# Performance work log

Hardware: AMD Instinct MI355X
Metric: run time of the kernel (lower is better)

Reference implementation:

```python
import jax, jax.numpy as jnp
import numpy as np

C, H_IMG = 1, 1024
N_PATCH = 64
L = 12          # blocks
NH = 12         # heads
D = 768         # hidden_d
DH = D // NH    # head dim
MLP = 4 * D
OUT_D = 1000
BATCH = 256
PATCH = H_IMG // N_PATCH
IN_D = C * PATCH
SEQ = N_PATCH + 1


def _pos_emb(pos, dim):
    # faithful to original: exponent uses i directly (2*i/dim), sin for even i, cos for odd i
    p = np.arange(pos, dtype=np.float64)[:, None]
    i = np.arange(dim, dtype=np.float64)[None, :]
    ang = p / np.power(10000.0, 2.0 * i / dim)
    pe = np.where((np.arange(dim)[None, :] % 2) == 0, np.sin(ang), np.cos(ang))
    return jnp.asarray(pe, dtype=jnp.float32)


def setup_inputs() -> dict:
    key = jax.random.key(0)
    ks = jax.random.split(key, 24)
    s = lambda fan: 1.0 / np.sqrt(fan)
    inp = {
        "images": jax.random.normal(ks[0], (BATCH, C, H_IMG), jnp.float32),
        "linear_w": jax.random.uniform(ks[1], (D, IN_D), jnp.float32, -s(IN_D), s(IN_D)),
        "linear_b": jax.random.uniform(ks[2], (D,), jnp.float32, -s(IN_D), s(IN_D)),
        "class_token": jax.random.uniform(ks[3], (1, D), jnp.float32),
        "pos_emb": _pos_emb(SEQ, D),
        "ln1_g": jnp.ones((L, D), jnp.float32),
        "ln1_b": jnp.zeros((L, D), jnp.float32),
        "wq": jax.random.uniform(ks[4], (L, NH, DH, DH), jnp.float32, -s(DH), s(DH)),
        "bq": jax.random.uniform(ks[5], (L, NH, DH), jnp.float32, -s(DH), s(DH)),
        "wk": jax.random.uniform(ks[6], (L, NH, DH, DH), jnp.float32, -s(DH), s(DH)),
        "bk": jax.random.uniform(ks[7], (L, NH, DH), jnp.float32, -s(DH), s(DH)),
        "wv": jax.random.uniform(ks[8], (L, NH, DH, DH), jnp.float32, -s(DH), s(DH)),
        "bv": jax.random.uniform(ks[9], (L, NH, DH), jnp.float32, -s(DH), s(DH)),
        "ln2_g": jnp.ones((L, D), jnp.float32),
        "ln2_b": jnp.zeros((L, D), jnp.float32),
        "w1": jax.random.uniform(ks[10], (L, MLP, D), jnp.float32, -s(D), s(D)),
        "b1": jax.random.uniform(ks[11], (L, MLP), jnp.float32, -s(D), s(D)),
        "w2": jax.random.uniform(ks[12], (L, D, MLP), jnp.float32, -s(MLP), s(MLP)),
        "b2": jax.random.uniform(ks[13], (L, D), jnp.float32, -s(MLP), s(MLP)),
        "head_w": jax.random.uniform(ks[14], (OUT_D, D), jnp.float32, -s(D), s(D)),
        "head_b": jax.random.uniform(ks[15], (OUT_D,), jnp.float32, -s(D), s(D)),
    }
    return inp


def _ln(x, g, b):
    m = jnp.mean(x, axis=-1, keepdims=True)
    v = jnp.var(x, axis=-1, keepdims=True)
    return (x - m) / jnp.sqrt(v + 1e-5) * g + b


def _block(x, g1, be1, wq, bq, wk, bk, wv, bv, g2, be2, w1, bb1, w2, bb2):
    B, S, _ = x.shape
    h = _ln(x, g1, be1).reshape(B, S, NH, DH)  # split heads along feature dim
    q = jnp.einsum('bshd,hed->bshe', h, wq) + bq
    k = jnp.einsum('bshd,hed->bshe', h, wk) + bk
    v = jnp.einsum('bshd,hed->bshe', h, wv) + bv
    scores = jnp.einsum('bshe,bthe->bhst', q, k) / np.sqrt(DH).astype(np.float32)
    attn = jax.nn.softmax(scores, axis=-1)
    o = jnp.einsum('bhst,bthe->bshe', attn, v).reshape(B, S, D)
    x = x + o
    h2 = _ln(x, g2, be2)
    m = jax.nn.gelu(jnp.einsum('bsd,fd->bsf', h2, w1) + bb1, approximate=False)
    m = jnp.einsum('bsf,df->bsd', m, w2) + bb2
    return x + m


def reference(images, linear_w, linear_b, class_token, pos_emb,
              ln1_g, ln1_b, wq, bq, wk, bk, wv, bv, ln2_g, ln2_b,
              w1, b1, w2, b2, head_w, head_b):
    n = images.shape[0]
    # patchify: [n, c, h] -> [n, n_patch, c*patch_size] (flatten is (c, patch) row-major)
    patches = images.reshape(n, C, N_PATCH, PATCH).transpose(0, 2, 1, 3).reshape(n, N_PATCH, IN_D)
    tokens = jnp.einsum('npi,di->npd', patches, linear_w) + linear_b
    cls = jnp.broadcast_to(class_token[None], (n, 1, D))
    x = jnp.concatenate([cls, tokens], axis=1) + pos_emb[None]
    for l in range(L):
        x = _block(x, ln1_g[l], ln1_b[l], wq[l], bq[l], wk[l], bk[l], wv[l], bv[l],
                   ln2_g[l], ln2_b[l], w1[l], b1[l], w2[l], b2[l])
    cls_out = x[:, 0]
    logits = cls_out @ head_w.T + head_b
    return jax.nn.softmax(logits, axis=-1)
```

## Files before the change

### kernel.cpp

```cpp
#include <hip/hip_runtime.h>

#define NLAYER 12
#define NHEAD  12
#define DHEAD  64
#define DMODEL 768
#define SEQL   65
#define NBATCH 256
#define MTOK   (NBATCH*SEQL)
#define MLPD   3072

typedef _Float16 f16;
typedef f16  f16x8 __attribute__((ext_vector_type(8)));
typedef f16  f16x4 __attribute__((ext_vector_type(4)));
typedef float f32x4 __attribute__((ext_vector_type(4)));

#define MFMA(a,b,c) __builtin_amdgcn_mfma_f32_16x16x32_f16(a,b,c,0,0,0)

__device__ __forceinline__ void gload16(const void* g, void* l) {
  __builtin_amdgcn_global_load_lds((const __attribute__((address_space(1))) void*)g,
                                   (__attribute__((address_space(3))) void*)l, 16, 0, 0);
}

__device__ __forceinline__ float gelu_f(float v) {
  float z = fabsf(v) * 0.70710678118654752f;
  float t = 1.f / (1.f + 0.3275911f * z);
  float p = ((((1.061405429f*t - 1.453152027f)*t + 1.421413741f)*t
              - 0.284496736f)*t + 0.254829592f)*t;
  float erfz = 1.f - p * __expf(-z*z);
  float erfv = copysignf(erfz, v);
  return 0.5f * v * (1.f + erfv);
}

__global__ __launch_bounds__(256) void cvt_f16k(const float* __restrict__ in,
                                                f16* __restrict__ out, int n) {
  long i = ((long)blockIdx.x*256 + threadIdx.x)*4;
  if (i >= n) return;
  const float4 v = *(const float4*)(in + i);
  f16x4 o = { (f16)v.x, (f16)v.y, (f16)v.z, (f16)v.w };
  *(f16x4*)(out + i) = o;
}

__global__ __launch_bounds__(256) void patch_embed(
    const float* __restrict__ images, const float* __restrict__ lw,
    const float* __restrict__ lb, const float* __restrict__ cls,
    const float* __restrict__ pe, float* __restrict__ x) {
  const int s = blockIdx.x, n = blockIdx.y, tid = threadIdx.x;
  __shared__ float p[16];
  if (s > 0 && tid < 16) p[tid] = images[(long)n*1024 + (s-1)*16 + tid];
  __syncthreads();
  float* xr = x + ((long)n*SEQL + s)*DMODEL;
  #pragma unroll
  for (int j = 0; j < 3; ++j) {
    int d = tid + j*256;
    float v;
    if (s == 0) {
      v = cls[d] + pe[d];
    } else {
      float acc = lb[d];
      #pragma unroll
      for (int i = 0; i < 16; ++i) acc += p[i]*lw[d*16+i];
      v = acc + pe[s*DMODEL + d];
    }
    xr[d] = v;
  }
}

__global__ __launch_bounds__(256) void ln_kernel(
    const float* __restrict__ x, const float* __restrict__ g,
    const float* __restrict__ b, f16* __restrict__ out) {
  const int row = blockIdx.x, tid = threadIdx.x;
  const float* xr = x + (long)row*DMODEL;
  float v0 = xr[tid], v1 = xr[tid+256], v2 = xr[tid+512];
  float s = v0+v1+v2;
  float s2 = v0*v0 + v1*v1 + v2*v2;
  #pragma unroll
  for (int o = 32; o >= 1; o >>= 1) { s += __shfl_xor(s, o); s2 += __shfl_xor(s2, o); }
  __shared__ float red[8];
  const int wave = tid>>6, lane = tid&63;
  if (lane == 0) { red[wave] = s; red[4+wave] = s2; }
  __syncthreads();
  s  = red[0]+red[1]+red[2]+red[3];
  s2 = red[4]+red[5]+red[6]+red[7];
  float mean = s * (1.f/768.f);
  float var  = s2 * (1.f/768.f) - mean*mean;
  float rstd = rsqrtf(var + 1e-5f);
  f16* orow = out + (long)row*DMODEL;
  orow[tid]     = (f16)((v0-mean)*rstd*g[tid]     + b[tid]);
  orow[tid+256] = (f16)((v1-mean)*rstd*g[tid+256] + b[tid+256]);
  orow[tid+512] = (f16)((v2-mean)*rstd*g[tid+512] + b[tid+512]);
}

__global__ __launch_bounds__(256) void attn_kernel(
    const f16* __restrict__ h, const f16* __restrict__ wq, const f16* __restrict__ wk,
    const f16* __restrict__ wv, const float* __restrict__ bq, const float* __restrict__ bk,
    const float* __restrict__ bv, float* __restrict__ x) {
  __shared__ __align__(16) f16 HsPs[80*104];
  __shared__ __align__(16) f16 Qs[80*72];
  __shared__ __align__(16) f16 Ks[80*72];
  __shared__ __align__(16) f16 Vt[64*104];
  const int hd = blockIdx.x, b = blockIdx.y;
  const int tid = threadIdx.x, wave = tid>>6, lane = tid&63;
  const int lc = lane & 15, lg = lane >> 4;
  const f16* hbase = h + ((long)b*SEQL)*DMODEL + hd*DHEAD;

  for (int c = tid; c < 80*8; c += 256) {
    int s = c >> 3, ec = (c & 7)*8;
    uint4 val = {0u,0u,0u,0u};
    if (s < SEQL) val = *(const uint4*)(hbase + (long)s*DMODEL + ec);
    *(uint4*)&HsPs[s*104 + ec] = val;
  }
  for (int c = tid; c < 64*104/8; c += 256) {
    uint4 z = {0u,0u,0u,0u};
    *(uint4*)&Vt[c*8] = z;
  }
  __syncthreads();

  for (int task = wave; task < 15; task += 4) {
    int mat = task / 5, mt = task % 5;
    const f16* W = (mat == 0 ? wq : mat == 1 ? wk : wv) + hd*DHEAD*DHEAD;
    const float* bias = (mat == 0 ? bq : mat == 1 ? bk : bv) + hd*DHEAD;
    #pragma unroll
    for (int nt = 0; nt < 4; ++nt) {
      f32x4 a = {0.f,0.f,0.f,0.f};
      #pragma unroll
      for (int kt = 0; kt < 2; ++kt) {
        f16x8 af = *(const f16x8*)&HsPs[(mt*16 + lc)*104 + kt*32 + lg*8];
        f16x8 bf = *(const f16x8*)&W[(nt*16 + lc)*DHEAD + kt*32 + lg*8];
        a = MFMA(af, bf, a);
      }
      float bb = bias[nt*16 + lc];
      #pragma unroll
      for (int r = 0; r < 4; ++r) {
        int s = mt*16 + lg*4 + r;
        int e = nt*16 + lc;
        float v = a[r] + bb;
        if (mat == 0)      Qs[s*72 + e] = (f16)v;
        else if (mat == 1) Ks[s*72 + e] = (f16)v;
        else               Vt[e*104 + s] = (f16)v;
      }
    }
  }
  __syncthreads();

  for (int mt = wave; mt < 5; mt += 4) {
    {
      uint2 z = {0u,0u};
      *(uint2*)&HsPs[(mt*16 + (lane>>2))*104 + 80 + (lane&3)*4] = z;
    }
    f32x4 sc[5];
    #pragma unroll
    for (int nt = 0; nt < 5; ++nt) {
      f32x4 a = {0.f,0.f,0.f,0.f};
      #pragma unroll
      for (int kt = 0; kt < 2; ++kt) {
        f16x8 af = *(const f16x8*)&Qs[(mt*16 + lc)*72 + kt*32 + lg*8];
        f16x8 bf = *(const f16x8*)&Ks[(nt*16 + lc)*72 + kt*32 + lg*8];
        a = MFMA(af, bf, a);
      }
      sc[nt] = a;
    }
    #pragma unroll
    for (int r = 0; r < 4; ++r) {
      float vals[5];
      #pragma unroll
      for (int nt = 0; nt < 5; ++nt) {
        float v = sc[nt][r]*0.125f;
        if (nt*16 + lc > 64) v = -1e30f;
        vals[nt] = v;
      }
      float mx = vals[0];
      #pragma unroll
      for (int nt = 1; nt < 5; ++nt) mx = fmaxf(mx, vals[nt]);
      #pragma unroll
      for (int o = 8; o >= 1; o >>= 1) mx = fmaxf(mx, __shfl_xor(mx, o, 16));
      float sum = 0.f, p[5];
      #pragma unroll
      for (int nt = 0; nt < 5; ++nt) { p[nt] = __expf(vals[nt]-mx); sum += p[nt]; }
      #pragma unroll
      for (int o = 8; o >= 1; o >>= 1) sum += __shfl_xor(sum, o, 16);
      float inv = 1.f/sum;
      int row = mt*16 + lg*4 + r;
      #pragma unroll
      for (int nt = 0; nt < 5; ++nt) HsPs[row*104 + nt*16 + lc] = (f16)(p[nt]*inv);
    }
    f32x4 oacc[4];
    #pragma unroll
    for (int nt = 0; nt < 4; ++nt) {
      f32x4 a = {0.f,0.f,0.f,0.f};
      #pragma unroll
      for (int kt = 0; kt < 3; ++kt) {
        f16x8 af = *(const f16x8*)&HsPs[(mt*16 + lc)*104 + kt*32 + lg*8];
        f16x8 bf = *(const f16x8*)&Vt[(nt*16 + lc)*104 + kt*32 + lg*8];
        a = MFMA(af, bf, a);
      }
      oacc[nt] = a;
    }
    float* xb = x + ((long)b*SEQL)*DMODEL + hd*DHEAD;
    #pragma unroll
    for (int nt = 0; nt < 4; ++nt) {
      #pragma unroll
      for (int r = 0; r < 4; ++r) {
        int s = mt*16 + lg*4 + r;
        if (s < SEQL) {
          int e = nt*16 + lc;
          xb[(long)s*DMODEL + e] += oacc[nt][r];
        }
      }
    }
  }
}

template<int ACT>
__global__ __launch_bounds__(512, 2) void gemm256(
    const f16* __restrict__ A, const f16* __restrict__ B,
    const float* __restrict__ bias, void* __restrict__ Cout,
    int M, int N, int K) {
  __shared__ __align__(16) f16 lds[65536];
  const int tid = threadIdx.x;
  const int wid = tid >> 6, lane = tid & 63;
  const int lrow = lane & 15, lk = lane >> 4;
  const int wr = wid >> 2, wc = wid & 3;

  const int gx = gridDim.x;
  const int nwg = gx * gridDim.y;
  const int orig = blockIdx.y * gx + blockIdx.x;
  const int q = nwg >> 3, r = nwg & 7;
  const int xcd = orig & 7, lin = orig >> 3;
  const int wgid = (xcd < r ? xcd*(q+1) : r*(q+1) + (xcd - r)*q) + lin;
  const int bx = wgid % gx, by = wgid / gx;

  const long m0 = (long)by * 256, n0 = (long)bx * 256;

  f32x4 acc[8][4];
  #pragma unroll
  for (int i = 0; i < 8; ++i)
    #pragma unroll
    for (int j = 0; j < 4; ++j) acc[i][j] = (f32x4){0.f,0.f,0.f,0.f};

  const int NT = K >> 5;
  auto stageA = [&](int t) {
    f16* As = &lds[(t & 3)*8192];
    #pragma unroll
    for (int i = 0; i < 2; ++i) {
      int c = tid + i*512;
      int row = c >> 2;
      int kp = (c & 3) ^ ((row >> 1) & 3);
      gload16(A + (m0 + row)*(long)K + t*32 + kp*8, &As[c*8]);
    }
  };
  auto stageB = [&](int t) {
    f16* Bs = &lds[32768 + (t & 3)*8192];
    #pragma unroll
    for (int i = 0; i < 2; ++i) {
      int c = tid + i*512;
      int row = c >> 2;
      int kp = (c & 3) ^ ((row >> 1) & 3);
      gload16(B + (n0 + row)*(long)K + t*32 + kp*8, &Bs[c*8]);
    }
  };

  stageA(0); stageB(0);
  stageA(1); stageB(1);
  stageA(2); stageB(2);

  for (int t = 0; t < NT; ++t) {
    const f16* As = &lds[(t & 3)*8192];
    const f16* Bs = &lds[32768 + (t & 3)*8192];
    {
      int rem = NT - 1 - t;
      if (rem >= 2)      asm volatile("s_waitcnt vmcnt(8)" ::: "memory");
      else if (rem == 1) asm volatile("s_waitcnt vmcnt(4)" ::: "memory");
      else               asm volatile("s_waitcnt vmcnt(0)" ::: "memory");
    }
    asm volatile("s_barrier" ::: "memory");

    if (t + 3 < NT) stageA(t + 3);
    f16x8 bf[4], af[4];
    #pragma unroll
    for (int nf = 0; nf < 4; ++nf) {
      int row = wc*64 + nf*16 + lrow;
      bf[nf] = *(const f16x8*)&Bs[row*32 + ((lk ^ ((row>>1)&3))*8)];
    }
    #pragma unroll
    for (int mf = 0; mf < 4; ++mf) {
      int row = wr*128 + mf*16 + lrow;
      af[mf] = *(const f16x8*)&As[row*32 + ((lk ^ ((row>>1)&3))*8)];
    }
    __builtin_amdgcn_s_setprio(1);
    #pragma unroll
    for (int mf = 0; mf < 4; ++mf)
      #pragma unroll
      for (int nf = 0; nf < 4; ++nf)
        acc[mf][nf] = MFMA(af[mf], bf[nf], acc[mf][nf]);
    __builtin_amdgcn_s_setprio(0);
    asm volatile("s_barrier" ::: "memory");

    if (t + 3 < NT) stageB(t + 3);
    #pragma unroll
    for (int mf = 0; mf < 4; ++mf) {
      int row = wr*128 + 64 + mf*16 + lrow;
      af[mf] = *(const f16x8*)&As[row*32 + ((lk ^ ((row>>1)&3))*8)];
    }
    __builtin_amdgcn_s_setprio(1);
    #pragma unroll
    for (int mf = 0; mf < 4; ++mf)
      #pragma unroll
      for (int nf = 0; nf < 4; ++nf)
        acc[4+mf][nf] = MFMA(af[mf], bf[nf], acc[4+mf][nf]);
    __builtin_amdgcn_s_setprio(0);
    asm volatile("s_barrier" ::: "memory");
  }

  if (ACT == 0) {
    #pragma unroll
    for (int nf = 0; nf < 4; ++nf) {
      int col = wc*64 + nf*16 + lrow;
      float bv = bias[(int)n0 + col];
      #pragma unroll
      for (int mf = 0; mf < 8; ++mf) {
        #pragma unroll
        for (int r2 = 0; r2 < 4; ++r2) {
          int row = wr*128 + mf*16 + lk*4 + r2;
          float v = acc[mf][nf][r2] + bv;
          int byte = (row*512 + col*2) ^ (((row>>2)&3)<<5);
          *(f16*)((char*)lds + byte) = (f16)gelu_f(v);
        }
      }
    }
    asm volatile("s_barrier" ::: "memory");
    f16* Cf = (f16*)Cout;
    #pragma unroll
    for (int i = 0; i < 16; ++i) {
      int g = i*512 + tid;
      int row = g >> 5, c5 = g & 31;
      int byte = (row*512 + c5*16) ^ (((row>>2)&3)<<5);
      f16x8 val = *(const f16x8*)((const char*)lds + byte);
      *(f16x8*)(Cf + (m0 + row)*(long)N + n0 + c5*8) = val;
    }
  } else {
    float* Cf = (float*)Cout;
    #pragma unroll
    for (int nf = 0; nf < 4; ++nf) {
      int col = (int)n0 + wc*64 + nf*16 + lrow;
      float bv = bias[col];
      #pragma unroll
      for (int mf = 0; mf < 8; ++mf) {
        #pragma unroll
        for (int r2 = 0; r2 < 4; ++r2) {
          long row = m0 + wr*128 + mf*16 + lk*4 + r2;
          Cf[row*(long)N + col] += acc[mf][nf][r2] + bv;
        }
      }
    }
  }
}

__global__ __launch_bounds__(256) void head_kernel(
    const float* __restrict__ x, const float* __restrict__ hw,
    const float* __restrict__ hb, float* __restrict__ out) {
  const int b = blockIdx.x, tid = threadIdx.x;
  __shared__ float cls[768];
  __shared__ float red[8];
  const float* xr = x + (long)b*SEQL*DMODEL;
  #pragma unroll
  for (int j = 0; j < 3; ++j) cls[tid + j*256] = xr[tid + j*256];
  __syncthreads();
  float lgv[4];
  #pragma unroll
  for (int j = 0; j < 4; ++j) {
    int c = tid + j*256;
    float acc = -1e30f;
    if (c < 1000) {
      const float* wr = hw + (long)c*768;
      float s_ = 0.f;
      for (int i = 0; i < 768; ++i) s_ += cls[i]*wr[i];
      acc = s_ + hb[c];
    }
    lgv[j] = acc;
  }
  const int wave = tid>>6, lane = tid&63;
  float mx = fmaxf(fmaxf(lgv[0],lgv[1]),fmaxf(lgv[2],lgv[3]));
  #pragma unroll
  for (int o = 32; o >= 1; o >>= 1) mx = fmaxf(mx, __shfl_xor(mx, o));
  if (lane == 0) red[wave] = mx;
  __syncthreads();
  mx = fmaxf(fmaxf(red[0],red[1]),fmaxf(red[2],red[3]));
  float e[4]; float sum = 0.f;
  #pragma unroll
  for (int j = 0; j < 4; ++j) {
    int c = tid + j*256;
    e[j] = (c < 1000) ? expf(lgv[j]-mx) : 0.f;
    sum += e[j];
  }
  #pragma unroll
  for (int o = 32; o >= 1; o >>= 1) sum += __shfl_xor(sum, o);
  if (lane == 0) red[4+wave] = sum;
  __syncthreads();
  sum = red[4]+red[5]+red[6]+red[7];
  float inv = 1.f/sum;
  #pragma unroll
  for (int j = 0; j < 4; ++j) {
    int c = tid + j*256;
    if (c < 1000) out[(long)b*1000 + c] = e[j]*inv;
  }
}

extern "C" void kernel_launch(void* const* d_in, const int* in_sizes, int n_in,
                              void* d_out, int out_size, void* d_ws, size_t ws_size,
                              hipStream_t stream) {
  const float* images     = (const float*)d_in[0];
  const float* linear_w   = (const float*)d_in[1];
  const float* linear_b   = (const float*)d_in[2];
  const float* class_tok  = (const float*)d_in[3];
  const float* pos_emb    = (const float*)d_in[4];
  const float* ln1_g      = (const float*)d_in[5];
  const float* ln1_b      = (const float*)d_in[6];
  const float* wq         = (const float*)d_in[7];
  const float* bq         = (const float*)d_in[8];
  const float* wk         = (const float*)d_in[9];
  const float* bk         = (const float*)d_in[10];
  const float* wv         = (const float*)d_in[11];
  const float* bv         = (const float*)d_in[12];
  const float* ln2_g      = (const float*)d_in[13];
  const float* ln2_b      = (const float*)d_in[14];
  const float* w1         = (const float*)d_in[15];
  const float* b1         = (const float*)d_in[16];
  const float* w2         = (const float*)d_in[17];
  const float* b2         = (const float*)d_in[18];
  const float* head_w     = (const float*)d_in[19];
  const float* head_b     = (const float*)d_in[20];

  char* ws = (char*)d_ws;
  float* xbuf = (float*)(ws + 0);
  f16*   hbuf = (f16*)(ws + 51118080);
  f16*   mbuf = (f16*)(ws + 76677120);
  f16*   w1all = (f16*)(ws + 178913280);
  f16*   w2all = (f16*)(ws + 235536384);
  f16*   wqbB  = (f16*)(ws + 292159488);
  f16*   wkbB  = (f16*)(ws + 293339136);
  f16*   wvbB  = (f16*)(ws + 294518784);
  f16*   w1b  = (f16*)(ws + 178913280);
  f16*   w2b  = (f16*)(ws + 183631872);
  f16*   wqbS = (f16*)(ws + 188350464);
  f16*   wkbS = (f16*)(ws + 189530112);
  f16*   wvbS = (f16*)(ws + 190709760);
  if (ws_size < 191889408ull) return;
  const bool big = ws_size >= 295698432ull;
  f16* wqb = big ? wqbB : wqbS;
  f16* wkb = big ? wkbB : wkbS;
  f16* wvb = big ? wvbB : wvbS;

  patch_embed<<<dim3(SEQL, NBATCH), 256, 0, stream>>>(images, linear_w, linear_b,
                                                      class_tok, pos_emb, xbuf);
  cvt_f16k<<<576, 256, 0, stream>>>(wq, wqb, 589824);
  cvt_f16k<<<576, 256, 0, stream>>>(wk, wkb, 589824);
  cvt_f16k<<<576, 256, 0, stream>>>(wv, wvb, 589824);
  if (big) {
    cvt_f16k<<<27648, 256, 0, stream>>>(w1, w1all, 28311552);
    cvt_f16k<<<27648, 256, 0, stream>>>(w2, w2all, 28311552);
  }

  for (int l = 0; l < NLAYER; ++l) {
    ln_kernel<<<MTOK, 256, 0, stream>>>(xbuf, ln1_g + l*768, ln1_b + l*768, hbuf);
    attn_kernel<<<dim3(NHEAD, NBATCH), 256, 0, stream>>>(
        hbuf, wqb + l*49152, wkb + l*49152, wvb + l*49152,
        bq + l*768, bk + l*768, bv + l*768, xbuf);
    ln_kernel<<<MTOK, 256, 0, stream>>>(xbuf, ln2_g + l*768, ln2_b + l*768, hbuf);
    f16* w1p = big ? (w1all + (long)l*2359296) : w1b;
    f16* w2p = big ? (w2all + (long)l*2359296) : w2b;
    if (!big) cvt_f16k<<<2304, 256, 0, stream>>>(w1 + (long)l*2359296, w1b, 2359296);
    gemm256<0><<<dim3(MLPD/256, MTOK/256), 512, 0, stream>>>(
        hbuf, w1p, b1 + l*3072, (void*)mbuf, MTOK, MLPD, DMODEL);
    if (!big) cvt_f16k<<<2304, 256, 0, stream>>>(w2 + (long)l*2359296, w2b, 2359296);
    gemm256<1><<<dim3(DMODEL/256, MTOK/256), 512, 0, stream>>>(
        mbuf, w2p, b2 + l*768, (void*)xbuf, MTOK, DMODEL, MLPD);
  }
  head_kernel<<<NBATCH, 256, 0, stream>>>(xbuf, head_w, head_b, (float*)d_out);
}
```

Baseline: 4.875 ms.

## Replace 256x256 MLP GEMM tile with 128x128 tile and 3-stage pipeline

Replaces the 512-thread 256x256-tile GEMM with a 256-thread 128x128-tile GEMM that has a 3-buffer LDS ring and a single barrier per K step. The goal is more workgroups, which matters for the N=768 second GEMM where the 256 tile gives only 3 column blocks, and higher occupancy through the smaller LDS footprint. The cost is lower data reuse per tile: each A/B element is loaded twice as often relative to the MFMA work. The prefetch distance also shrinks from three stages to two.

```diff
diff --git a/kernel.cpp b/kernel.cpp
--- a/kernel.cpp
+++ b/kernel.cpp
@@ -211,15 +211,15 @@
 }
 
 template<int ACT>
-__global__ __launch_bounds__(512, 2) void gemm256(
+__global__ __launch_bounds__(256, 3) void gemm128(
     const f16* __restrict__ A, const f16* __restrict__ B,
     const float* __restrict__ bias, void* __restrict__ Cout,
     int M, int N, int K) {
-  __shared__ __align__(16) f16 lds[65536];
+  __shared__ __align__(16) f16 lds[24576];
   const int tid = threadIdx.x;
-  const int wid = tid >> 6, lane = tid & 63;
+  const int wave = tid >> 6, lane = tid & 63;
   const int lrow = lane & 15, lk = lane >> 4;
-  const int wr = wid >> 2, wc = wid & 3;
+  const int wm = (wave >> 1) * 64, wn = (wave & 1) * 64;
 
   const int gx = gridDim.x;
   const int nwg = gx * gridDim.y;
@@ -229,125 +229,97 @@
   const int wgid = (xcd < r ? xcd*(q+1) : r*(q+1) + (xcd - r)*q) + lin;
   const int bx = wgid % gx, by = wgid / gx;
 
-  const long m0 = (long)by * 256, n0 = (long)bx * 256;
-
-  f32x4 acc[8][4];
-  #pragma unroll
-  for (int i = 0; i < 8; ++i)
+  const long m0 = (long)by * 128, n0 = (long)bx * 128;
+
+  f32x4 acc[4][4];
+  #pragma unroll
+  for (int i = 0; i < 4; ++i)
     #pragma unroll
     for (int j = 0; j < 4; ++j) acc[i][j] = (f32x4){0.f,0.f,0.f,0.f};
 
   const int NT = K >> 5;
-  auto stageA = [&](int t) {
-    f16* As = &lds[(t & 3)*8192];
+  auto stage = [&](int t) {
+    const int s = t % 3;
+    f16* As = &lds[s*4096];
+    f16* Bs = &lds[12288 + s*4096];
     #pragma unroll
     for (int i = 0; i < 2; ++i) {
-      int c = tid + i*512;
+      int c = tid + i*256;
       int row = c >> 2;
       int kp = (c & 3) ^ ((row >> 1) & 3);
       gload16(A + (m0 + row)*(long)K + t*32 + kp*8, &As[c*8]);
+      gload16(B + (n0 + row)*(long)K + t*32 + kp*8, &Bs[c*8]);
     }
   };
-  auto stageB = [&](int t) {
-    f16* Bs = &lds[32768 + (t & 3)*8192];
-    #pragma unroll
-    for (int i = 0; i < 2; ++i) {
-      int c = tid + i*512;
-      int row = c >> 2;
-      int kp = (c & 3) ^ ((row >> 1) & 3);
-      gload16(B + (n0 + row)*(long)K + t*32 + kp*8, &Bs[c*8]);
-    }
-  };
-
-  stageA(0); stageB(0);
-  stageA(1); stageB(1);
-  stageA(2); stageB(2);
+  stage(0); stage(1);
 
   for (int t = 0; t < NT; ++t) {
-    const f16* As = &lds[(t & 3)*8192];
-    const f16* Bs = &lds[32768 + (t & 3)*8192];
-    {
-      int rem = NT - 1 - t;
-      if (rem >= 2)      asm volatile("s_waitcnt vmcnt(8)" ::: "memory");
-      else if (rem == 1) asm volatile("s_waitcnt vmcnt(4)" ::: "memory");
-      else               asm volatile("s_waitcnt vmcnt(0)" ::: "memory");
-    }
+    const int s = t % 3;
+    const f16* As = &lds[s*4096];
+    const f16* Bs = &lds[12288 + s*4096];
+    if (t + 1 < NT) asm volatile("s_waitcnt vmcnt(4)" ::: "memory");
+    else            asm volatile("s_waitcnt vmcnt(0)" ::: "memory");
     asm volatile("s_barrier" ::: "memory");
-
-    if (t + 3 < NT) stageA(t + 3);
-    f16x8 bf[4], af[4];
+    if (t + 2 < NT) stage(t + 2);
+    f16x8 af[4], bfr[4];
+    #pragma unroll
+    for (int mf = 0; mf < 4; ++mf) {
+      int row = wm + mf*16 + lrow;
+      af[mf] = *(const f16x8*)&As[row*32 + ((lk ^ ((row>>1)&3))*8)];
+    }
     #pragma unroll
     for (int nf = 0; nf < 4; ++nf) {
-      int row = wc*64 + nf*16 + lrow;
-      bf[nf] = *(const f16x8*)&Bs[row*32 + ((lk ^ ((row>>1)&3))*8)];
-    }
-    #pragma unroll
-    for (int mf = 0; mf < 4; ++mf) {
-      int row = wr*128 + mf*16 + lrow;
-      af[mf] = *(const f16x8*)&As[row*32 + ((lk ^ ((row>>1)&3))*8)];
+      int row = wn + nf*16 + lrow;
+      bfr[nf] = *(const f16x8*)&Bs[row*32 + ((lk ^ ((row>>1)&3))*8)];
     }
     __builtin_amdgcn_s_setprio(1);
     #pragma unroll
     for (int mf = 0; mf < 4; ++mf)
       #pragma unroll
       for (int nf = 0; nf < 4; ++nf)
-        acc[mf][nf] = MFMA(af[mf], bf[nf], acc[mf][nf]);
+        acc[mf][nf] = MFMA(af[mf], bfr[nf], acc[mf][nf]);
     __builtin_amdgcn_s_setprio(0);
-    asm volatile("s_barrier" ::: "memory");
-
-    if (t + 3 < NT) stageB(t + 3);
-    #pragma unroll
-    for (int mf = 0; mf < 4; ++mf) {
-      int row = wr*128 + 64 + mf*16 + lrow;
-      af[mf] = *(const f16x8*)&As[row*32 + ((lk ^ ((row>>1)&3))*8)];
-    }
-    __builtin_amdgcn_s_setprio(1);
-    #pragma unroll
-    for (int mf = 0; mf < 4; ++mf)
-      #pragma unroll
-      for (int nf = 0; nf < 4; ++nf)
-        acc[4+mf][nf] = MFMA(af[mf], bf[nf], acc[4+mf][nf]);
-    __builtin_amdgcn_s_setprio(0);
-    asm volatile("s_barrier" ::: "memory");
-  }
+  }
+
+  __syncthreads();
 
   if (ACT == 0) {
     #pragma unroll
     for (int nf = 0; nf < 4; ++nf) {
-      int col = wc*64 + nf*16 + lrow;
+      int col = wn + nf*16 + lrow;
       float bv = bias[(int)n0 + col];
       #pragma unroll
-      for (int mf = 0; mf < 8; ++mf) {
+      for (int mf = 0; mf < 4; ++mf) {
         #pragma unroll
         for (int r2 = 0; r2 < 4; ++r2) {
-          int row = wr*128 + mf*16 + lk*4 + r2;
+          int row = wm + mf*16 + lk*4 + r2;
           float v = acc[mf][nf][r2] + bv;
-          int byte = (row*512 + col*2) ^ (((row>>2)&3)<<5);
+          int byte = (row*256 + col*2) ^ (((row>>2)&7)<<4);
           *(f16*)((char*)lds + byte) = (f16)gelu_f(v);
         }
       }
     }
-    asm volatile("s_barrier" ::: "memory");
+    __syncthreads();
     f16* Cf = (f16*)Cout;
     #pragma unroll
-    for (int i = 0; i < 16; ++i) {
-      int g = i*512 + tid;
-      int row = g >> 5, c5 = g & 31;
-      int byte = (row*512 + c5*16) ^ (((row>>2)&3)<<5);
+    for (int i = 0; i < 8; ++i) {
+      int g = i*256 + tid;
+      int row = g >> 4, ch = g & 15;
+      int byte = (row*256 + ch*16) ^ (((row>>2)&7)<<4);
       f16x8 val = *(const f16x8*)((const char*)lds + byte);
-      *(f16x8*)(Cf + (m0 + row)*(long)N + n0 + c5*8) = val;
+      *(f16x8*)(Cf + (m0 + row)*(long)N + n0 + ch*8) = val;
     }
   } else {
     float* Cf = (float*)Cout;
     #pragma unroll
     for (int nf = 0; nf < 4; ++nf) {
-      int col = (int)n0 + wc*64 + nf*16 + lrow;
+      int col = (int)n0 + wn + nf*16 + lrow;
       float bv = bias[col];
       #pragma unroll
-      for (int mf = 0; mf < 8; ++mf) {
+      for (int mf = 0; mf < 4; ++mf) {
         #pragma unroll
         for (int r2 = 0; r2 < 4; ++r2) {
-          long row = m0 + wr*128 + mf*16 + lk*4 + r2;
+          long row = m0 + wm + mf*16 + lk*4 + r2;
           Cf[row*(long)N + col] += acc[mf][nf][r2] + bv;
         }
       }
@@ -469,10 +441,10 @@
     f16* w1p = big ? (w1all + (long)l*2359296) : w1b;
     f16* w2p = big ? (w2all + (long)l*2359296) : w2b;
     if (!big) cvt_f16k<<<2304, 256, 0, stream>>>(w1 + (long)l*2359296, w1b, 2359296);
-    gemm256<0><<<dim3(MLPD/256, MTOK/256), 512, 0, stream>>>(
+    gemm128<0><<<dim3(MLPD/128, MTOK/128), 256, 0, stream>>>(
         hbuf, w1p, b1 + l*3072, (void*)mbuf, MTOK, MLPD, DMODEL);
     if (!big) cvt_f16k<<<2304, 256, 0, stream>>>(w2 + (long)l*2359296, w2b, 2359296);
-    gemm256<1><<<dim3(DMODEL/256, MTOK/256), 512, 0, stream>>>(
+    gemm128<1><<<dim3(DMODEL/128, MTOK/128), 256, 0, stream>>>(
         mbuf, w2p, b2 + l*768, (void*)xbuf, MTOK, DMODEL, MLPD);
   }
   head_kernel<<<NBATCH, 256, 0, stream>>>(xbuf, head_w, head_b, (float*)d_out);
```

After: 4.706 ms. -3.5%, faster.

## Restructure MLP GEMM to double-buffered BK=64 pipeline with fragment-ordered LDS layout

Applied to the files above, without the earlier changes.

Reworks the MLP GEMM main loop. The old 4-stage ring of 32-wide K tiles becomes a 2-slot double buffer of 64-wide K tiles. Global-to-LDS loads now write tiles in MFMA-fragment order, with precomputed per-thread offsets, so LDS reads are contiguous per lane and need no XOR swizzle. The loop is split into four quarter phases that interleave prefetch issue with MFMA work. This aims to cut barrier and waitcnt overhead per K step and improve LDS read efficiency, but the shallower prefetch depth may expose more global load latency. The GELU epilogue staging swizzle is also changed.

```diff
diff --git a/kernel.cpp b/kernel.cpp
--- a/kernel.cpp
+++ b/kernel.cpp
@@ -211,22 +211,22 @@
 }
 
 template<int ACT>
-__global__ __launch_bounds__(512, 2) void gemm256(
+__global__ __launch_bounds__(512, 2) void gemmQ(
     const f16* __restrict__ A, const f16* __restrict__ B,
     const float* __restrict__ bias, void* __restrict__ Cout,
     int M, int N, int K) {
   __shared__ __align__(16) f16 lds[65536];
   const int tid = threadIdx.x;
   const int wid = tid >> 6, lane = tid & 63;
-  const int lrow = lane & 15, lk = lane >> 4;
+  const int lr = lane & 15, lg4 = lane >> 4;
   const int wr = wid >> 2, wc = wid & 3;
 
   const int gx = gridDim.x;
   const int nwg = gx * gridDim.y;
   const int orig = blockIdx.y * gx + blockIdx.x;
-  const int q = nwg >> 3, r = nwg & 7;
+  const int q8 = nwg >> 3, r8 = nwg & 7;
   const int xcd = orig & 7, lin = orig >> 3;
-  const int wgid = (xcd < r ? xcd*(q+1) : r*(q+1) + (xcd - r)*q) + lin;
+  const int wgid = (xcd < r8 ? xcd*(q8+1) : r8*(q8+1) + (xcd - r8)*q8) + lin;
   const int bx = wgid % gx, by = wgid / gx;
 
   const long m0 = (long)by * 256, n0 = (long)bx * 256;
@@ -237,117 +237,114 @@
     #pragma unroll
     for (int j = 0; j < 4; ++j) acc[i][j] = (f32x4){0.f,0.f,0.f,0.f};
 
-  const int NT = K >> 5;
-  auto stageA = [&](int t) {
-    f16* As = &lds[(t & 3)*8192];
-    #pragma unroll
-    for (int i = 0; i < 2; ++i) {
-      int c = tid + i*512;
-      int row = c >> 2;
-      int kp = (c & 3) ^ ((row >> 1) & 3);
-      gload16(A + (m0 + row)*(long)K + t*32 + kp*8, &As[c*8]);
-    }
+  const int NT = K >> 6;
+
+  int off[4];
+  #pragma unroll
+  for (int i = 0; i < 4; ++i) {
+    int c = tid + i*512;
+    int fr = c >> 7, ks = (c >> 6) & 1, l = c & 63;
+    off[i] = (fr*16 + (l & 15))*K + ks*32 + (l >> 4)*8;
+  }
+  const f16* Abase = A + m0*K;
+  const f16* Bbase = B + n0*K;
+
+  auto stageA = [&](const f16* Ab, int slot) {
+    f16* dst = &lds[slot*32768];
+    #pragma unroll
+    for (int i = 0; i < 4; ++i) gload16(Ab + off[i], &dst[(tid + i*512)*8]);
   };
-  auto stageB = [&](int t) {
-    f16* Bs = &lds[32768 + (t & 3)*8192];
-    #pragma unroll
-    for (int i = 0; i < 2; ++i) {
-      int c = tid + i*512;
-      int row = c >> 2;
-      int kp = (c & 3) ^ ((row >> 1) & 3);
-      gload16(B + (n0 + row)*(long)K + t*32 + kp*8, &Bs[c*8]);
-    }
+  auto stageB = [&](const f16* Bb, int slot) {
+    f16* dst = &lds[slot*32768 + 16384];
+    #pragma unroll
+    for (int i = 0; i < 4; ++i) gload16(Bb + off[i], &dst[(tid + i*512)*8]);
   };
 
-  stageA(0); stageB(0);
-  stageA(1); stageB(1);
-  stageA(2); stageB(2);
-
+  stageA(Abase, 0); stageB(Bbase, 0);
+  Abase += 64; Bbase += 64;
+  asm volatile("s_waitcnt vmcnt(0)" ::: "memory");
+  asm volatile("s_barrier" ::: "memory");
+
+  const int laneoff = lane*8;
+  int slot = 0;
   for (int t = 0; t < NT; ++t) {
-    const f16* As = &lds[(t & 3)*8192];
-    const f16* Bs = &lds[32768 + (t & 3)*8192];
-    {
-      int rem = NT - 1 - t;
-      if (rem >= 2)      asm volatile("s_waitcnt vmcnt(8)" ::: "memory");
-      else if (rem == 1) asm volatile("s_waitcnt vmcnt(4)" ::: "memory");
-      else               asm volatile("s_waitcnt vmcnt(0)" ::: "memory");
-    }
-    asm volatile("s_barrier" ::: "memory");
-
-    if (t + 3 < NT) stageA(t + 3);
-    f16x8 bf[4], af[4];
+    const f16* As = &lds[slot*32768];
+    const f16* Bs = As + 16384;
+    const bool pf = (t + 1) < NT;
+    f16x8 bf[4][2];
+    #pragma unroll
+    for (int qp = 0; qp < 4; ++qp) {
+      if (qp == 0) {
+        #pragma unroll
+        for (int nf = 0; nf < 4; ++nf)
+          #pragma unroll
+          for (int ks = 0; ks < 2; ++ks)
+            bf[nf][ks] = *(const f16x8*)&Bs[((wc*4 + nf)*2 + ks)*512 + laneoff];
+      }
+      f16x8 af[2][2];
+      #pragma unroll
+      for (int j = 0; j < 2; ++j)
+        #pragma unroll
+        for (int ks = 0; ks < 2; ++ks)
+          af[j][ks] = *(const f16x8*)&As[((wr*8 + qp*2 + j)*2 + ks)*512 + laneoff];
+      if (pf) {
+        if (qp == 0) stageA(Abase, slot ^ 1);
+        else if (qp == 1) stageB(Bbase, slot ^ 1);
+      }
+      asm volatile("s_barrier" ::: "memory");
+      __builtin_amdgcn_s_setprio(1);
+      #pragma unroll
+      for (int j = 0; j < 2; ++j)
+        #pragma unroll
+        for (int nf = 0; nf < 4; ++nf) {
+          acc[qp*2+j][nf] = MFMA(af[j][0], bf[nf][0], acc[qp*2+j][nf]);
+          acc[qp*2+j][nf] = MFMA(af[j][1], bf[nf][1], acc[qp*2+j][nf]);
+        }
+      __builtin_amdgcn_s_setprio(0);
+      if (qp == 3 && pf) asm volatile("s_waitcnt vmcnt(0)" ::: "memory");
+      asm volatile("s_barrier" ::: "memory");
+    }
+    if (pf) { Abase += 64; Bbase += 64; }
+    slot ^= 1;
+  }
+
+  if (ACT == 0) {
+    char* Ct = (char*)lds;
     #pragma unroll
     for (int nf = 0; nf < 4; ++nf) {
-      int row = wc*64 + nf*16 + lrow;
-      bf[nf] = *(const f16x8*)&Bs[row*32 + ((lk ^ ((row>>1)&3))*8)];
-    }
-    #pragma unroll
-    for (int mf = 0; mf < 4; ++mf) {
-      int row = wr*128 + mf*16 + lrow;
-      af[mf] = *(const f16x8*)&As[row*32 + ((lk ^ ((row>>1)&3))*8)];
-    }
-    __builtin_amdgcn_s_setprio(1);
-    #pragma unroll
-    for (int mf = 0; mf < 4; ++mf)
-      #pragma unroll
-      for (int nf = 0; nf < 4; ++nf)
-        acc[mf][nf] = MFMA(af[mf], bf[nf], acc[mf][nf]);
-    __builtin_amdgcn_s_setprio(0);
-    asm volatile("s_barrier" ::: "memory");
-
-    if (t + 3 < NT) stageB(t + 3);
-    #pragma unroll
-    for (int mf = 0; mf < 4; ++mf) {
-      int row = wr*128 + 64 + mf*16 + lrow;
-      af[mf] = *(const f16x8*)&As[row*32 + ((lk ^ ((row>>1)&3))*8)];
-    }
-    __builtin_amdgcn_s_setprio(1);
-    #pragma unroll
-    for (int mf = 0; mf < 4; ++mf)
-      #pragma unroll
-      for (int nf = 0; nf < 4; ++nf)
-        acc[4+mf][nf] = MFMA(af[mf], bf[nf], acc[4+mf][nf]);
-    __builtin_amdgcn_s_setprio(0);
-    asm volatile("s_barrier" ::: "memory");
-  }
-
-  if (ACT == 0) {
-    #pragma unroll
-    for (int nf = 0; nf < 4; ++nf) {
-      int col = wc*64 + nf*16 + lrow;
+      int col = wc*64 + nf*16 + lr;
       float bv = bias[(int)n0 + col];
       #pragma unroll
       for (int mf = 0; mf < 8; ++mf) {
         #pragma unroll
         for (int r2 = 0; r2 < 4; ++r2) {
-          int row = wr*128 + mf*16 + lk*4 + r2;
-          float v = acc[mf][nf][r2] + bv;
-          int byte = (row*512 + col*2) ^ (((row>>2)&3)<<5);
-          *(f16*)((char*)lds + byte) = (f16)gelu_f(v);
+          int row = wr*128 + mf*16 + lg4*4 + r2;
+          int byte = row*512 + ((col*2) ^ ((row & 15) << 4));
+          *(f16*)(Ct + byte) = (f16)gelu_f(acc[mf][nf][r2] + bv);
         }
       }
     }
-    asm volatile("s_barrier" ::: "memory");
+    __syncthreads();
     f16* Cf = (f16*)Cout;
     #pragma unroll
     for (int i = 0; i < 16; ++i) {
       int g = i*512 + tid;
-      int row = g >> 5, c5 = g & 31;
-      int byte = (row*512 + c5*16) ^ (((row>>2)&3)<<5);
-      f16x8 val = *(const f16x8*)((const char*)lds + byte);
-      *(f16x8*)(Cf + (m0 + row)*(long)N + n0 + c5*8) = val;
+      int row = g >> 5, ch = g & 31;
+      int byte = row*512 + ((ch ^ (row & 15)) << 4);
+      f16x8 val = *(const f16x8*)(Ct + byte);
+      *(f16x8*)(Cf + (m0 + row)*(long)N + n0 + ch*8) = val;
     }
   } else {
     float* Cf = (float*)Cout;
     #pragma unroll
     for (int nf = 0; nf < 4; ++nf) {
-      int col = (int)n0 + wc*64 + nf*16 + lrow;
+      int col = (int)n0 + wc*64 + nf*16 + lr;
       float bv = bias[col];
       #pragma unroll
       for (int mf = 0; mf < 8; ++mf) {
         #pragma unroll
         for (int r2 = 0; r2 < 4; ++r2) {
-          long row = m0 + wr*128 + mf*16 + lk*4 + r2;
+          long row = m0 + wr*128 + mf*16 + lg4*4 + r2;
           Cf[row*(long)N + col] += acc[mf][nf][r2] + bv;
         }
       }
@@ -469,10 +466,10 @@
     f16* w1p = big ? (w1all + (long)l*2359296) : w1b;
     f16* w2p = big ? (w2all + (long)l*2359296) : w2b;
     if (!big) cvt_f16k<<<2304, 256, 0, stream>>>(w1 + (long)l*2359296, w1b, 2359296);
-    gemm256<0><<<dim3(MLPD/256, MTOK/256), 512, 0, stream>>>(
+    gemmQ<0><<<dim3(MLPD/256, MTOK/256), 512, 0, stream>>>(
         hbuf, w1p, b1 + l*3072, (void*)mbuf, MTOK, MLPD, DMODEL);
     if (!big) cvt_f16k<<<2304, 256, 0, stream>>>(w2 + (long)l*2359296, w2b, 2359296);
-    gemm256<1><<<dim3(DMODEL/256, MTOK/256), 512, 0, stream>>>(
+    gemmQ<1><<<dim3(DMODEL/256, MTOK/256), 512, 0, stream>>>(
         mbuf, w2p, b2 + l*768, (void*)xbuf, MTOK, DMODEL, MLPD);
   }
   head_kernel<<<NBATCH, 256, 0, stream>>>(xbuf, head_w, head_b, (float*)d_out);
```

New measurement: 5.374 ms. 10.2% more time.
